# Performance work log

Measured on AMD Instinct MI355X. Metric: run time of the kernel, lower is better.

Reference implementation:

```python
import jax, jax.numpy as jnp
import numpy as np

N = 50000      # nodes per graph
E = 800000     # edges per graph (avg degree 16)
IN = 128       # in_channels == hidden_channels
HID = 128      # out_channels (heads=1)
R = 8          # num_relations
NEG = 0.2      # PyG RGATConv default negative_slope


def setup_inputs() -> dict:
    key = jax.random.key(0)
    ks = jax.random.split(key, 14)
    s_w = (2.0 / (IN + HID)) ** 0.5  # glorot-ish scale
    return {
        "x_one": jax.random.normal(ks[0], (N, IN), jnp.float32),
        "edge_index_one": jax.random.randint(ks[1], (2, E), 0, N),
        "edge_type_one": jax.random.randint(ks[2], (E,), 0, R),
        "x_two": jax.random.normal(ks[3], (N, IN), jnp.float32),
        "edge_index_two": jax.random.randint(ks[4], (2, E), 0, N),
        "edge_type_two": jax.random.randint(ks[5], (E,), 0, R),
        "W1": jax.random.normal(ks[6], (R, IN, HID), jnp.float32) * s_w,
        "q1": jax.random.normal(ks[7], (HID, 1), jnp.float32) * s_w,
        "k1": jax.random.normal(ks[8], (HID, 1), jnp.float32) * s_w,
        "b1": jnp.zeros((HID,), jnp.float32),
        "W2": jax.random.normal(ks[9], (R, IN, HID), jnp.float32) * s_w,
        "q2": jax.random.normal(ks[10], (HID, 1), jnp.float32) * s_w,
        "k2": jax.random.normal(ks[11], (HID, 1), jnp.float32) * s_w,
        "b2": jnp.zeros((HID,), jnp.float32),
    }


def _rgat(x, edge_index, edge_type, W, q, k, b):
    """PyG RGATConv (heads=1, additive-self-attention, across-relation)."""
    n = x.shape[0]
    src, dst = edge_index[0], edge_index[1]
    # per-relation linear transform of all nodes: [R, N, HID]
    xt = jnp.einsum('nd,rdo->rno', x, W)
    out_i = xt[edge_type, dst]   # [E, HID] transformed target (x_i W_r)
    out_j = xt[edge_type, src]   # [E, HID] transformed source (x_j W_r)
    qi = out_i @ q               # [E, 1]
    kj = out_j @ k               # [E, 1]
    alpha = jax.nn.leaky_relu(qi + kj, NEG)
    # scatter-softmax over incoming edges of each dst node
    amax = jax.ops.segment_max(alpha, dst, num_segments=n)
    amax = jnp.where(jnp.isfinite(amax), amax, 0.0)
    ex = jnp.exp(alpha - amax[dst])
    denom = jax.ops.segment_sum(ex, dst, num_segments=n) + 1e-16
    a = ex / denom[dst]          # [E, 1]
    # weighted scatter-add aggregation + bias
    out = jax.ops.segment_sum(a * out_j, dst, num_segments=n) + b
    return out


def reference(x_one, edge_index_one, edge_type_one,
              x_two, edge_index_two, edge_type_two,
              W1, q1, k1, b1, W2, q2, k2, b2):
    o1 = jax.nn.relu(_rgat(x_one, edge_index_one, edge_type_one, W1, q1, k1, b1))
    o2 = jax.nn.relu(_rgat(x_two, edge_index_two, edge_type_two, W2, q2, k2, b2))
    return (o1, o2)
```

## Files before the change

### kernel.cpp

```cpp
#include <hip/hip_runtime.h>


typedef unsigned short u16;
typedef __attribute__((ext_vector_type(8))) short short8;
typedef __attribute__((ext_vector_type(4))) float floatx4;
typedef __attribute__((ext_vector_type(4))) float float4v;
typedef __attribute__((ext_vector_type(4))) unsigned uint4v;

#define BCAP 8192

__device__ __forceinline__ u16 f2bf(float f) {
  union { float f; unsigned u; } v; v.f = f;
  unsigned r = v.u + 0x7FFFu + ((v.u >> 16) & 1u);
  return (u16)(r >> 16);
}
__device__ __forceinline__ float bflo(unsigned v) {
  union { unsigned u; float f; } c; c.u = v << 16; return c.f;
}
__device__ __forceinline__ float bfhi(unsigned v) {
  union { unsigned u; float f; } c; c.u = v & 0xffff0000u; return c.f;
}
__device__ __forceinline__ unsigned cvtpk(float lo, float hi) {
  unsigned r;
  asm("v_cvt_pk_bf16_f32 %0, %1, %2" : "=v"(r) : "v"(lo), "v"(hi));
  return r;
}

__global__ void __launch_bounds__(256) k_prep(
    const float* __restrict__ W1, const float* __restrict__ q1,
    const float* __restrict__ k1, const float* __restrict__ W2,
    const float* __restrict__ q2, const float* __restrict__ k2,
    u16* __restrict__ Wb, u16* __restrict__ Bqk, int* __restrict__ bcnt,
    int KK, int wbHalf) {
  int b = blockIdx.x, tid = threadIdx.x;
  int wbBlocks = 2 * wbHalf;
  if (b < wbBlocks) {
    int gy = b >= wbHalf;
    int t = (b - gy * wbHalf) * 256 + tid;
    int lane = t & 63, nt = (t >> 6) & 7, kk = t >> 9;
    if (kk >= KK) return;
    const float* W = gy ? W2 : W1;
    u16* out = Wb + (size_t)gy * KK * 4096;
    int q = lane >> 4, m16 = lane & 15;
    int c = nt * 16 + m16;
    short8 v;
#pragma unroll
    for (int j = 0; j < 8; ++j) {
      int k = kk * 32 + q * 8 + j;
      v[j] = (short)f2bf(W[(size_t)k * 128 + c]);
    }
    *(short8*)(out + (size_t)t * 8) = v;
  } else {
    int bb = b - wbBlocks;
    if (bb < 2) {
      int z = bb * 256 + tid;
      bcnt[z] = 0;
    }
    int idx = bb * 256 + tid;
    int j = idx & 7, lane = (idx >> 3) & 63, kk = (idx >> 9) & 3, g = idx >> 11;
    int k = kk * 32 + ((lane >> 4) & 3) * 8 + j;
    int n = lane & 15;
    const float* W = g ? W2 : W1;
    const float* vec = (n < 8) ? (g ? q2 : q1) : (g ? k2 : k1);
    const float* row = W + ((size_t)(n & 7) * 128 + k) * 128;
    float s = 0.f;
#pragma unroll
    for (int o = 0; o < 128; o += 4) {
      float4v wv = *(const float4v*)(row + o);
      float4v qv = *(const float4v*)(vec + o);
      s += wv.x * qv.x + wv.y * qv.y + wv.z * qv.z + wv.w * qv.w;
    }
    Bqk[idx] = f2bf(s);
  }
}

struct BinSmem {
  int hist[512];
  int basev[512];
  int runstart[512];
  unsigned sta[8192];
};
union SortGemmSmem {
  BinSmem bn;
  u16 st[4][2][2048];
};

__global__ void __launch_bounds__(256) k_sortgemm(
    const int* __restrict__ ei1, const int* __restrict__ et1,
    const int* __restrict__ ei2, const int* __restrict__ et2,
    int* __restrict__ bcnt, uint2* __restrict__ staged,
    const float* __restrict__ x, const u16* __restrict__ Wb,
    const u16* __restrict__ Bqk, u16* __restrict__ xt,
    float* __restrict__ sq, float* __restrict__ sk,
    int N, int E, int NB, int R, int nbin, int gx) {
  __shared__ SortGemmSmem sm;
  int tid = threadIdx.x;

  if ((int)blockIdx.x < nbin) {
    int* hist = sm.bn.hist;
    int* basev = sm.bn.basev;
    int* runstart = sm.bn.runstart;
    unsigned* sta = sm.bn.sta;
    int E2 = 2 * E;
    int e0 = blockIdx.x * 4096;
    int cnt2 = min(4096, E2 - e0);
    for (int i = tid; i < 512; i += 256) hist[i] = 0;
    __syncthreads();
    int dstg[16], srcet[16], rank[16];
#pragma unroll
    for (int j = 0; j < 16; ++j) {
      int e = e0 + j * 256 + tid;
      dstg[j] = -1;
      if (e < E2) {
        int g = e >= E;
        int el = e - (g ? E : 0);
        const int* ei = g ? ei2 : ei1;
        int s = ei[el], d = ei[E + el];
        int etv = (g ? et2 : et1)[el];
        dstg[j] = g * N + d;
        srcet[j] = (s << 3) | etv;
        rank[j] = atomicAdd(&hist[dstg[j] >> 8], 1);
      }
    }
    __syncthreads();
    basev[tid] = hist[tid];
    basev[tid + 256] = hist[tid + 256];
    __syncthreads();
    for (int off = 1; off < 512; off <<= 1) {
      int i0 = tid, i1 = tid + 256;
      int v0 = (i0 >= off) ? basev[i0 - off] : 0;
      int v1 = (i1 >= off) ? basev[i1 - off] : 0;
      __syncthreads();
      basev[i0] += v0; basev[i1] += v1;
      __syncthreads();
    }
    for (int i = tid; i < NB; i += 256)
      if (hist[i] > 0) runstart[i] = atomicAdd(&bcnt[i], hist[i]);
    __syncthreads();
#pragma unroll
    for (int j = 0; j < 16; ++j)
      if (dstg[j] >= 0) {
        int b = dstg[j] >> 8;
        int slot = basev[b] - hist[b] + rank[j];
        sta[slot * 2] = (unsigned)dstg[j];
        sta[slot * 2 + 1] = (unsigned)srcet[j];
      }
    __syncthreads();
    for (int i = tid; i < cnt2; i += 256) {
      unsigned dg = sta[i * 2], se = sta[i * 2 + 1];
      int b = (int)(dg >> 8);
      int dest = (b << 13) + runstart[b] + (i - (basev[b] - hist[b]));
      staged[dest] = make_uint2(dg, se);
    }
    return;
  }

  int f = blockIdx.x - nbin;
  int bx = f % gx;
  int by = f / gx;
  int wave = tid >> 6, lane = tid & 63;
  int m0 = bx * 64 + wave * 16;
  int rbase = by * 4;
  int q = lane >> 4, m16 = lane & 15;
  int node = m0 + m16;
  int srow = (node < N) ? node : N - 1;
  short8 bfrag[4];
#pragma unroll
  for (int kk = 0; kk < 4; ++kk) {
    const float* ap = x + (size_t)srow * 128 + kk * 32 + q * 8;
    float4v f0 = *(const float4v*)ap;
    float4v f1 = *(const float4v*)(ap + 4);
    union { unsigned u[4]; short8 s; } pb;
    pb.u[0] = cvtpk(f0.x, f0.y); pb.u[1] = cvtpk(f0.z, f0.w);
    pb.u[2] = cvtpk(f1.x, f1.y); pb.u[3] = cvtpk(f1.z, f1.w);
    bfrag[kk] = pb.s;
  }
  if (by == 0) {
    floatx4 accq = (floatx4){0.f, 0.f, 0.f, 0.f};
#pragma unroll
    for (int kk = 0; kk < 4; ++kk) {
      short8 aq = *(const short8*)(Bqk + (size_t)kk * 512 + lane * 8);
      accq = __builtin_amdgcn_mfma_f32_16x16x32_bf16(aq, bfrag[kk], accq, 0, 0, 0);
    }
    if (node < N) {
      float* dst = (q < 2 ? sq : sk) + (size_t)node * 8 + (q & 1) * 4;
      *(float4v*)dst = (float4v){accq[0], accq[1], accq[2], accq[3]};
    }
  }
#pragma unroll
  for (int rr = 0; rr < 4; ++rr) {
    int r = rbase + rr;
    u16* s = sm.st[wave][rr & 1];
    floatx4 acc[8];
#pragma unroll
    for (int nt = 0; nt < 8; ++nt) acc[nt] = (floatx4){0.f, 0.f, 0.f, 0.f};
#pragma unroll
    for (int kk = 0; kk < 4; ++kk) {
      const u16* wbp = Wb + ((size_t)((r * 4 + kk) * 8) * 64 + lane) * 8;
#pragma unroll
      for (int nt = 0; nt < 8; ++nt) {
        short8 a = *(const short8*)(wbp + nt * 512);
        acc[nt] = __builtin_amdgcn_mfma_f32_16x16x32_bf16(a, bfrag[kk], acc[nt], 0, 0, 0);
      }
    }
#pragma unroll
    for (int nt = 0; nt < 8; ++nt) {
      union { unsigned u[2]; unsigned long long ull; } pk;
      pk.u[0] = cvtpk(acc[nt][0], acc[nt][1]);
      pk.u[1] = cvtpk(acc[nt][2], acc[nt][3]);
      int c16 = 2 * nt + (q >> 1);
      *(unsigned long long*)(s + (((m16 << 4) + (c16 ^ m16)) << 3) + ((q & 1) << 2)) = pk.ull;
    }
#pragma unroll
    for (int it = 0; it < 4; ++it) {
      int rl = it * 4 + q;
      int gm = m0 + rl;
      if (gm < N) {
        uint4v vv = *(const uint4v*)(s + (((rl << 4) + (m16 ^ rl)) << 3));
        *(uint4v*)(xt + ((size_t)r * N + gm) * 128 + m16 * 8) = vv;
      }
    }
  }
}

__global__ void __launch_bounds__(256) k_scatter3(
    const uint2* __restrict__ staged, const int* __restrict__ bcnt,
    int* __restrict__ offs, int* __restrict__ ends, int* __restrict__ csr,
    int N2) {
  __shared__ int hist[256];
  __shared__ int sd[256];
  __shared__ int cur[256];
  int b = blockIdx.x, tid = threadIdx.x;
  int nb0 = b << 8;
  int nnode = min(256, N2 - nb0);
  int s0 = b << 13;
  int cnt = bcnt[b];
  hist[tid] = 0;
  __syncthreads();
  for (int i = tid; i < cnt; i += 256)
    atomicAdd(&hist[(int)staged[s0 + i].x - nb0], 1);
  __syncthreads();
  int v = hist[tid];
  sd[tid] = v; __syncthreads();
  for (int off = 1; off < 256; off <<= 1) {
    int t = (tid >= off) ? sd[tid - off] : 0;
    __syncthreads();
    sd[tid] += t;
    __syncthreads();
  }
  int ex = sd[tid] - v;
  if (tid < nnode) {
    offs[nb0 + tid] = s0 + ex;
    ends[nb0 + tid] = s0 + ex + v;
  }
  cur[tid] = ex;
  __syncthreads();
  for (int i = tid; i < cnt; i += 256) {
    uint2 en = staged[s0 + i];
    int node = (int)en.x - nb0;
    int sl = atomicAdd(&cur[node], 1);
    csr[s0 + sl] = (int)en.y;
  }
}

__global__ void __launch_bounds__(256) k_gemm_xt(
    const float* __restrict__ x, const u16* __restrict__ Wb,
    const u16* __restrict__ Bqk, u16* __restrict__ xt,
    float* __restrict__ sq, float* __restrict__ sk,
    int N, int R, int node_base) {
  __shared__ u16 st[4][2][2048];
  int wave = threadIdx.x >> 6, lane = threadIdx.x & 63;
  int m0 = blockIdx.x * 64 + wave * 16;
  int rbase = blockIdx.y * 4;
  int q = lane >> 4, m16 = lane & 15;
  int node = m0 + m16;
  int srow = (node < N) ? node : N - 1;
  short8 bfrag[4];
#pragma unroll
  for (int kk = 0; kk < 4; ++kk) {
    const float* ap = x + (size_t)srow * 128 + kk * 32 + q * 8;
    float4v f0 = *(const float4v*)ap;
    float4v f1 = *(const float4v*)(ap + 4);
    union { unsigned u[4]; short8 s; } pb;
    pb.u[0] = cvtpk(f0.x, f0.y); pb.u[1] = cvtpk(f0.z, f0.w);
    pb.u[2] = cvtpk(f1.x, f1.y); pb.u[3] = cvtpk(f1.z, f1.w);
    bfrag[kk] = pb.s;
  }
  if (blockIdx.y == 0) {
    floatx4 accq = (floatx4){0.f, 0.f, 0.f, 0.f};
#pragma unroll
    for (int kk = 0; kk < 4; ++kk) {
      short8 aq = *(const short8*)(Bqk + (size_t)kk * 512 + lane * 8);
      accq = __builtin_amdgcn_mfma_f32_16x16x32_bf16(aq, bfrag[kk], accq, 0, 0, 0);
    }
    if (node < N) {
      float* dst = (q < 2 ? sq : sk) + (size_t)(node_base + node) * 8 + (q & 1) * 4;
      *(float4v*)dst = (float4v){accq[0], accq[1], accq[2], accq[3]};
    }
  }
#pragma unroll
  for (int rr = 0; rr < 4; ++rr) {
    int r = rbase + rr;
    u16* s = st[wave][rr & 1];
    floatx4 acc[8];
#pragma unroll
    for (int nt = 0; nt < 8; ++nt) acc[nt] = (floatx4){0.f, 0.f, 0.f, 0.f};
#pragma unroll
    for (int kk = 0; kk < 4; ++kk) {
      const u16* wbp = Wb + ((size_t)((r * 4 + kk) * 8) * 64 + lane) * 8;
#pragma unroll
      for (int nt = 0; nt < 8; ++nt) {
        short8 a = *(const short8*)(wbp + nt * 512);
        acc[nt] = __builtin_amdgcn_mfma_f32_16x16x32_bf16(a, bfrag[kk], acc[nt], 0, 0, 0);
      }
    }
#pragma unroll
    for (int nt = 0; nt < 8; ++nt) {
      union { unsigned u[2]; unsigned long long ull; } pk;
      pk.u[0] = cvtpk(acc[nt][0], acc[nt][1]);
      pk.u[1] = cvtpk(acc[nt][2], acc[nt][3]);
      int c16 = 2 * nt + (q >> 1);
      *(unsigned long long*)(s + (((m16 << 4) + (c16 ^ m16)) << 3) + ((q & 1) << 2)) = pk.ull;
    }
#pragma unroll
    for (int it = 0; it < 4; ++it) {
      int rl = it * 4 + q;
      int gm = m0 + rl;
      if (gm < N) {
        uint4v vv = *(const uint4v*)(s + (((rl << 4) + (m16 ^ rl)) << 3));
        *(uint4v*)(xt + ((size_t)r * N + gm) * 128 + m16 * 8) = vv;
      }
    }
  }
}

__global__ void __launch_bounds__(256) k_aggregate(
    const int* __restrict__ csr, const int* __restrict__ offs,
    const int* __restrict__ ends,
    const float* __restrict__ sq, const float* __restrict__ sk,
    const u16* __restrict__ xt, const float* __restrict__ bias,
    float* __restrict__ out, int N, int node_base) {
  int nl = blockIdx.x * 4 + (threadIdx.x >> 6);
  int lane = threadIdx.x & 63;
  if (nl >= N) return;
  int node = node_base + nl;
  int start = offs[node], end = ends[node];
  const float* sqn = sq + (size_t)node * 8;

  float al[8]; int pl[8];
  float m = -INFINITY;
  {
    int c = 0;
    for (int i = start + lane; i < end; i += 64, ++c) {
      int p = csr[i]; int s = p >> 3, e = p & 7;
      float a = sqn[e] + sk[(size_t)(node_base + s) * 8 + e];
      a = (a > 0.f) ? a : 0.2f * a;
      if (c < 8) { al[c] = a; pl[c] = p; }
      m = fmaxf(m, a);
    }
  }
#pragma unroll
  for (int off = 32; off; off >>= 1) m = fmaxf(m, __shfl_xor(m, off));

  float ssum = 0.f;
  {
    int c = 0;
    for (int i = start + lane; i < end; i += 64, ++c) {
      float a;
      if (c < 8) a = al[c];
      else {
        int p = csr[i]; int s = p >> 3, e = p & 7;
        a = sqn[e] + sk[(size_t)(node_base + s) * 8 + e];
        a = (a > 0.f) ? a : 0.2f * a;
      }
      ssum += __expf(a - m);
    }
  }
#pragma unroll
  for (int off = 32; off; off >>= 1) ssum += __shfl_xor(ssum, off);
  float inv = 1.f / (ssum + 1e-16f);

  float acc0 = 0.f, acc1 = 0.f;
  const char* xtb = (const char*)xt;
  int c = 0;
  for (int base = start; base < end; base += 64, ++c) {
    int cnt = min(64, end - base);
    float w = 0.f; int b = 0;
    {
      int i = base + lane;
      if (i < end) {
        int p; float a;
        if (c < 8) { p = pl[c]; a = al[c]; }
        else {
          p = csr[i]; int s = p >> 3, e = p & 7;
          a = sqn[e] + sk[(size_t)(node_base + s) * 8 + e];
          a = (a > 0.f) ? a : 0.2f * a;
        }
        w = __expf(a - m) * inv;
        b = ((p & 7) * N + (p >> 3)) << 8;
      }
    }
    int j = 0;
    for (; j + 3 < cnt; j += 4) {
      float w0 = __shfl(w, j), w1 = __shfl(w, j + 1),
            w2 = __shfl(w, j + 2), w3 = __shfl(w, j + 3);
      int b0 = __shfl(b, j), b1 = __shfl(b, j + 1),
          b2 = __shfl(b, j + 2), b3 = __shfl(b, j + 3);
      unsigned v0 = *(const unsigned*)(xtb + b0 + lane * 4);
      unsigned v1 = *(const unsigned*)(xtb + b1 + lane * 4);
      unsigned v2 = *(const unsigned*)(xtb + b2 + lane * 4);
      unsigned v3 = *(const unsigned*)(xtb + b3 + lane * 4);
      acc0 += w0 * bflo(v0); acc1 += w0 * bfhi(v0);
      acc0 += w1 * bflo(v1); acc1 += w1 * bfhi(v1);
      acc0 += w2 * bflo(v2); acc1 += w2 * bfhi(v2);
      acc0 += w3 * bflo(v3); acc1 += w3 * bfhi(v3);
    }
    for (; j < cnt; ++j) {
      float w0 = __shfl(w, j);
      int b0 = __shfl(b, j);
      unsigned v0 = *(const unsigned*)(xtb + b0 + lane * 4);
      acc0 += w0 * bflo(v0); acc1 += w0 * bfhi(v0);
    }
  }
  float o0 = fmaxf(acc0 + bias[lane * 2], 0.f);
  float o1 = fmaxf(acc1 + bias[lane * 2 + 1], 0.f);
  union { float f[2]; unsigned long long u; } pk;
  pk.f[0] = o0; pk.f[1] = o1;
  __builtin_nontemporal_store(pk.u,
      (unsigned long long*)(out + (size_t)nl * 128 + lane * 2));
}

extern "C" void kernel_launch(void* const* d_in, const int* in_sizes, int n_in,
                              void* d_out, int out_size, void* d_ws, size_t ws_size,
                              hipStream_t stream) {
  const float* x1 = (const float*)d_in[0];
  const int* ei1 = (const int*)d_in[1];
  const int* et1 = (const int*)d_in[2];
  const float* x2 = (const float*)d_in[3];
  const int* ei2 = (const int*)d_in[4];
  const int* et2 = (const int*)d_in[5];
  const float* W1 = (const float*)d_in[6];
  const float* q1 = (const float*)d_in[7];
  const float* k1 = (const float*)d_in[8];
  const float* b1 = (const float*)d_in[9];
  const float* W2 = (const float*)d_in[10];
  const float* q2 = (const float*)d_in[11];
  const float* k2 = (const float*)d_in[12];
  const float* b2 = (const float*)d_in[13];

  const int N = in_sizes[0] / 128;
  const int E = in_sizes[1] / 2;
  const int R = in_sizes[6] / (128 * 128);
  const int KK = R * 4;
  const int N2 = 2 * N;
  const int NB = (N2 + 255) >> 8;

  size_t off = 0;
  char* w = (char*)d_ws;
  auto carve = [&](size_t bytes) -> void* {
    void* p = w + off;
    off += (bytes + 255) & ~(size_t)255;
    return p;
  };
  u16* Wb = (u16*)carve((size_t)2 * KK * 4096 * 2);
  u16* Bqk = (u16*)carve((size_t)2 * 4 * 64 * 8 * 2);
  float* sq = (float*)carve((size_t)N2 * 8 * 4);
  float* sk = (float*)carve((size_t)N2 * 8 * 4);
  int* offs = (int*)carve((size_t)N2 * 4);
  int* ends = (int*)carve((size_t)N2 * 4);
  int* bcnt = (int*)carve(512 * 4);
  int* csr = (int*)carve((size_t)NB * BCAP * 4);
  uint2* staged = (uint2*)carve((size_t)NB * BCAP * 8);
  u16* xt = (u16*)carve((size_t)R * N * 128 * 2);
  if (off > ws_size) return;

  const int nbin = (2 * E + 4095) / 4096;
  const int gx = (N + 63) / 64;
  const int wbHalf = (KK * 512 + 255) / 256;

  k_prep<<<dim3(2 * wbHalf + 16), dim3(256), 0, stream>>>(
      W1, q1, k1, W2, q2, k2, Wb, Bqk, bcnt, KK, wbHalf);
  k_sortgemm<<<dim3(nbin + 2 * gx), dim3(256), 0, stream>>>(
      ei1, et1, ei2, et2, bcnt, staged,
      x1, Wb, Bqk, xt, sq, sk, N, E, NB, R, nbin, gx);
  k_scatter3<<<dim3(NB), dim3(256), 0, stream>>>(staged, bcnt, offs, ends, csr, N2);
  k_aggregate<<<dim3((N + 3) / 4), dim3(256), 0, stream>>>(
      csr, offs, ends, sq, sk, xt, b1, (float*)d_out, N, 0);
  k_gemm_xt<<<dim3(gx, 2), dim3(256), 0, stream>>>(
      x2, Wb + (size_t)KK * 4096, Bqk + 2048, xt, sq, sk, N, R, N);
  k_aggregate<<<dim3((N + 3) / 4), dim3(256), 0, stream>>>(
      csr, offs, ends, sq, sk, xt, b2,
      (float*)d_out + (size_t)N * 128, N, N);
}
```

Measured before the change: 324.2 us.

## Overlap graph-two GEMM with graph-one aggregation in a combined launch

The GEMM and aggregation bodies move into shared device functions, and a new combined kernel runs the graph-two per-relation transform blocks alongside the graph-one aggregation blocks. The graph-two xt buffer is placed where the staging buffer was, which is free once scatter has finished, so the two stages no longer serialise on one buffer. This saves one launch and lets compute-bound MFMA work overlap the memory-bound gather. If the workspace is too small it falls back to the old sequential path.

```diff
diff --git a/kernel.cpp b/kernel.cpp
--- a/kernel.cpp
+++ b/kernel.cpp
@@ -85,6 +85,171 @@
   u16 st[4][2][2048];
 };
 
+__device__ __forceinline__ void gemm_body(
+    u16 st[4][2][2048], int bx, int by, int tid,
+    const float* __restrict__ x, const u16* __restrict__ Wb,
+    const u16* __restrict__ Bqk, u16* __restrict__ xt,
+    float* __restrict__ sq, float* __restrict__ sk,
+    int N, int node_base) {
+  int wave = tid >> 6, lane = tid & 63;
+  int m0 = bx * 64 + wave * 16;
+  int rbase = by * 4;
+  int q = lane >> 4, m16 = lane & 15;
+  int node = m0 + m16;
+  int srow = (node < N) ? node : N - 1;
+  short8 bfrag[4];
+#pragma unroll
+  for (int kk = 0; kk < 4; ++kk) {
+    const float* ap = x + (size_t)srow * 128 + kk * 32 + q * 8;
+    float4v f0 = *(const float4v*)ap;
+    float4v f1 = *(const float4v*)(ap + 4);
+    union { unsigned u[4]; short8 s; } pb;
+    pb.u[0] = cvtpk(f0.x, f0.y); pb.u[1] = cvtpk(f0.z, f0.w);
+    pb.u[2] = cvtpk(f1.x, f1.y); pb.u[3] = cvtpk(f1.z, f1.w);
+    bfrag[kk] = pb.s;
+  }
+  if (by == 0) {
+    floatx4 accq = (floatx4){0.f, 0.f, 0.f, 0.f};
+#pragma unroll
+    for (int kk = 0; kk < 4; ++kk) {
+      short8 aq = *(const short8*)(Bqk + (size_t)kk * 512 + lane * 8);
+      accq = __builtin_amdgcn_mfma_f32_16x16x32_bf16(aq, bfrag[kk], accq, 0, 0, 0);
+    }
+    if (node < N) {
+      float* dst = (q < 2 ? sq : sk) + (size_t)(node_base + node) * 8 + (q & 1) * 4;
+      *(float4v*)dst = (float4v){accq[0], accq[1], accq[2], accq[3]};
+    }
+  }
+#pragma unroll
+  for (int rr = 0; rr < 4; ++rr) {
+    int r = rbase + rr;
+    u16* s = st[tid >> 6][rr & 1];
+    floatx4 acc[8];
+#pragma unroll
+    for (int nt = 0; nt < 8; ++nt) acc[nt] = (floatx4){0.f, 0.f, 0.f, 0.f};
+#pragma unroll
+    for (int kk = 0; kk < 4; ++kk) {
+      const u16* wbp = Wb + ((size_t)((r * 4 + kk) * 8) * 64 + lane) * 8;
+#pragma unroll
+      for (int nt = 0; nt < 8; ++nt) {
+        short8 a = *(const short8*)(wbp + nt * 512);
+        acc[nt] = __builtin_amdgcn_mfma_f32_16x16x32_bf16(a, bfrag[kk], acc[nt], 0, 0, 0);
+      }
+    }
+#pragma unroll
+    for (int nt = 0; nt < 8; ++nt) {
+      union { unsigned u[2]; unsigned long long ull; } pk;
+      pk.u[0] = cvtpk(acc[nt][0], acc[nt][1]);
+      pk.u[1] = cvtpk(acc[nt][2], acc[nt][3]);
+      int c16 = 2 * nt + (q >> 1);
+      *(unsigned long long*)(s + (((m16 << 4) + (c16 ^ m16)) << 3) + ((q & 1) << 2)) = pk.ull;
+    }
+#pragma unroll
+    for (int it = 0; it < 4; ++it) {
+      int rl = it * 4 + q;
+      int gm = m0 + rl;
+      if (gm < N) {
+        uint4v vv = *(const uint4v*)(s + (((rl << 4) + (m16 ^ rl)) << 3));
+        *(uint4v*)(xt + ((size_t)r * N + gm) * 128 + m16 * 8) = vv;
+      }
+    }
+  }
+}
+
+__device__ __forceinline__ void agg_body(
+    int nl, int lane,
+    const int* __restrict__ csr, const int* __restrict__ offs,
+    const int* __restrict__ ends,
+    const float* __restrict__ sq, const float* __restrict__ sk,
+    const u16* __restrict__ xt, const float* __restrict__ bias,
+    float* __restrict__ out, int N, int node_base) {
+  int node = node_base + nl;
+  int start = offs[node], end = ends[node];
+  const float* sqn = sq + (size_t)node * 8;
+
+  float al[8]; int pl[8];
+  float m = -INFINITY;
+  {
+    int c = 0;
+    for (int i = start + lane; i < end; i += 64, ++c) {
+      int p = csr[i]; int s = p >> 3, e = p & 7;
+      float a = sqn[e] + sk[(size_t)(node_base + s) * 8 + e];
+      a = (a > 0.f) ? a : 0.2f * a;
+      if (c < 8) { al[c] = a; pl[c] = p; }
+      m = fmaxf(m, a);
+    }
+  }
+#pragma unroll
+  for (int off = 32; off; off >>= 1) m = fmaxf(m, __shfl_xor(m, off));
+
+  float ssum = 0.f;
+  {
+    int c = 0;
+    for (int i = start + lane; i < end; i += 64, ++c) {
+      float a;
+      if (c < 8) a = al[c];
+      else {
+        int p = csr[i]; int s = p >> 3, e = p & 7;
+        a = sqn[e] + sk[(size_t)(node_base + s) * 8 + e];
+        a = (a > 0.f) ? a : 0.2f * a;
+      }
+      ssum += __expf(a - m);
+    }
+  }
+#pragma unroll
+  for (int off = 32; off; off >>= 1) ssum += __shfl_xor(ssum, off);
+  float inv = 1.f / (ssum + 1e-16f);
+
+  float acc0 = 0.f, acc1 = 0.f;
+  const char* xtb = (const char*)xt;
+  int c = 0;
+  for (int base = start; base < end; base += 64, ++c) {
+    int cnt = min(64, end - base);
+    float w = 0.f; int b = 0;
+    {
+      int i = base + lane;
+      if (i < end) {
+        int p; float a;
+        if (c < 8) { p = pl[c]; a = al[c]; }
+        else {
+          p = csr[i]; int s = p >> 3, e = p & 7;
+          a = sqn[e] + sk[(size_t)(node_base + s) * 8 + e];
+          a = (a > 0.f) ? a : 0.2f * a;
+        }
+        w = __expf(a - m) * inv;
+        b = ((p & 7) * N + (p >> 3)) << 8;
+      }
+    }
+    int j = 0;
+    for (; j + 3 < cnt; j += 4) {
+      float w0 = __shfl(w, j), w1 = __shfl(w, j + 1),
+            w2 = __shfl(w, j + 2), w3 = __shfl(w, j + 3);
+      int b0 = __shfl(b, j), b1 = __shfl(b, j + 1),
+          b2 = __shfl(b, j + 2), b3 = __shfl(b, j + 3);
+      unsigned v0 = *(const unsigned*)(xtb + b0 + lane * 4);
+      unsigned v1 = *(const unsigned*)(xtb + b1 + lane * 4);
+      unsigned v2 = *(const unsigned*)(xtb + b2 + lane * 4);
+      unsigned v3 = *(const unsigned*)(xtb + b3 + lane * 4);
+      acc0 += w0 * bflo(v0); acc1 += w0 * bfhi(v0);
+      acc0 += w1 * bflo(v1); acc1 += w1 * bfhi(v1);
+      acc0 += w2 * bflo(v2); acc1 += w2 * bfhi(v2);
+      acc0 += w3 * bflo(v3); acc1 += w3 * bfhi(v3);
+    }
+    for (; j < cnt; ++j) {
+      float w0 = __shfl(w, j);
+      int b0 = __shfl(b, j);
+      unsigned v0 = *(const unsigned*)(xtb + b0 + lane * 4);
+      acc0 += w0 * bflo(v0); acc1 += w0 * bfhi(v0);
+    }
+  }
+  float o0 = fmaxf(acc0 + bias[lane * 2], 0.f);
+  float o1 = fmaxf(acc1 + bias[lane * 2 + 1], 0.f);
+  union { float f[2]; unsigned long long u; } pk;
+  pk.f[0] = o0; pk.f[1] = o1;
+  __builtin_nontemporal_store(pk.u,
+      (unsigned long long*)(out + (size_t)nl * 128 + lane * 2));
+}
+
 __global__ void __launch_bounds__(256) k_sortgemm(
     const int* __restrict__ ei1, const int* __restrict__ et1,
     const int* __restrict__ ei2, const int* __restrict__ et2,
@@ -154,73 +319,8 @@
     }
     return;
   }
-
   int f = blockIdx.x - nbin;
-  int bx = f % gx;
-  int by = f / gx;
-  int wave = tid >> 6, lane = tid & 63;
-  int m0 = bx * 64 + wave * 16;
-  int rbase = by * 4;
-  int q = lane >> 4, m16 = lane & 15;
-  int node = m0 + m16;
-  int srow = (node < N) ? node : N - 1;
-  short8 bfrag[4];
-#pragma unroll
-  for (int kk = 0; kk < 4; ++kk) {
-    const float* ap = x + (size_t)srow * 128 + kk * 32 + q * 8;
-    float4v f0 = *(const float4v*)ap;
-    float4v f1 = *(const float4v*)(ap + 4);
-    union { unsigned u[4]; short8 s; } pb;
-    pb.u[0] = cvtpk(f0.x, f0.y); pb.u[1] = cvtpk(f0.z, f0.w);
-    pb.u[2] = cvtpk(f1.x, f1.y); pb.u[3] = cvtpk(f1.z, f1.w);
-    bfrag[kk] = pb.s;
-  }
-  if (by == 0) {
-    floatx4 accq = (floatx4){0.f, 0.f, 0.f, 0.f};
-#pragma unroll
-    for (int kk = 0; kk < 4; ++kk) {
-      short8 aq = *(const short8*)(Bqk + (size_t)kk * 512 + lane * 8);
-      accq = __builtin_amdgcn_mfma_f32_16x16x32_bf16(aq, bfrag[kk], accq, 0, 0, 0);
-    }
-    if (node < N) {
-      float* dst = (q < 2 ? sq : sk) + (size_t)node * 8 + (q & 1) * 4;
-      *(float4v*)dst = (float4v){accq[0], accq[1], accq[2], accq[3]};
-    }
-  }
-#pragma unroll
-  for (int rr = 0; rr < 4; ++rr) {
-    int r = rbase + rr;
-    u16* s = sm.st[wave][rr & 1];
-    floatx4 acc[8];
-#pragma unroll
-    for (int nt = 0; nt < 8; ++nt) acc[nt] = (floatx4){0.f, 0.f, 0.f, 0.f};
-#pragma unroll
-    for (int kk = 0; kk < 4; ++kk) {
-      const u16* wbp = Wb + ((size_t)((r * 4 + kk) * 8) * 64 + lane) * 8;
-#pragma unroll
-      for (int nt = 0; nt < 8; ++nt) {
-        short8 a = *(const short8*)(wbp + nt * 512);
-        acc[nt] = __builtin_amdgcn_mfma_f32_16x16x32_bf16(a, bfrag[kk], acc[nt], 0, 0, 0);
-      }
-    }
-#pragma unroll
-    for (int nt = 0; nt < 8; ++nt) {
-      union { unsigned u[2]; unsigned long long ull; } pk;
-      pk.u[0] = cvtpk(acc[nt][0], acc[nt][1]);
-      pk.u[1] = cvtpk(acc[nt][2], acc[nt][3]);
-      int c16 = 2 * nt + (q >> 1);
-      *(unsigned long long*)(s + (((m16 << 4) + (c16 ^ m16)) << 3) + ((q & 1) << 2)) = pk.ull;
-    }
-#pragma unroll
-    for (int it = 0; it < 4; ++it) {
-      int rl = it * 4 + q;
-      int gm = m0 + rl;
-      if (gm < N) {
-        uint4v vv = *(const uint4v*)(s + (((rl << 4) + (m16 ^ rl)) << 3));
-        *(uint4v*)(xt + ((size_t)r * N + gm) * 128 + m16 * 8) = vv;
-      }
-    }
-  }
+  gemm_body(sm.st, f % gx, f / gx, tid, x, Wb, Bqk, xt, sq, sk, N, 0);
 }
 
 __global__ void __launch_bounds__(256) k_scatter3(
@@ -263,75 +363,36 @@
   }
 }
 
+__global__ void __launch_bounds__(256) k_aggemm(
+    const int* __restrict__ csr, const int* __restrict__ offs,
+    const int* __restrict__ ends,
+    const float* __restrict__ sq, const float* __restrict__ sk,
+    const u16* __restrict__ xt0, const float* __restrict__ b1,
+    float* __restrict__ out,
+    const float* __restrict__ x2, const u16* __restrict__ Wb1,
+    const u16* __restrict__ Bqk1, u16* __restrict__ xt1,
+    float* __restrict__ sqw, float* __restrict__ skw,
+    int N, int R, int gx) {
+  __shared__ u16 st[4][2][2048];
+  int tid = threadIdx.x;
+  if ((int)blockIdx.x < 2 * gx) {
+    int f = blockIdx.x;
+    gemm_body(st, f % gx, f / gx, tid, x2, Wb1, Bqk1, xt1, sqw, skw, N, N);
+    return;
+  }
+  int nl = (blockIdx.x - 2 * gx) * 4 + (tid >> 6);
+  if (nl >= N) return;
+  agg_body(nl, tid & 63, csr, offs, ends, sq, sk, xt0, b1, out, N, 0);
+}
+
 __global__ void __launch_bounds__(256) k_gemm_xt(
     const float* __restrict__ x, const u16* __restrict__ Wb,
     const u16* __restrict__ Bqk, u16* __restrict__ xt,
     float* __restrict__ sq, float* __restrict__ sk,
     int N, int R, int node_base) {
   __shared__ u16 st[4][2][2048];
-  int wave = threadIdx.x >> 6, lane = threadIdx.x & 63;
-  int m0 = blockIdx.x * 64 + wave * 16;
-  int rbase = blockIdx.y * 4;
-  int q = lane >> 4, m16 = lane & 15;
-  int node = m0 + m16;
-  int srow = (node < N) ? node : N - 1;
-  short8 bfrag[4];
-#pragma unroll
-  for (int kk = 0; kk < 4; ++kk) {
-    const float* ap = x + (size_t)srow * 128 + kk * 32 + q * 8;
-    float4v f0 = *(const float4v*)ap;
-    float4v f1 = *(const float4v*)(ap + 4);
-    union { unsigned u[4]; short8 s; } pb;
-    pb.u[0] = cvtpk(f0.x, f0.y); pb.u[1] = cvtpk(f0.z, f0.w);
-    pb.u[2] = cvtpk(f1.x, f1.y); pb.u[3] = cvtpk(f1.z, f1.w);
-    bfrag[kk] = pb.s;
-  }
-  if (blockIdx.y == 0) {
-    floatx4 accq = (floatx4){0.f, 0.f, 0.f, 0.f};
-#pragma unroll
-    for (int kk = 0; kk < 4; ++kk) {
-      short8 aq = *(const short8*)(Bqk + (size_t)kk * 512 + lane * 8);
-      accq = __builtin_amdgcn_mfma_f32_16x16x32_bf16(aq, bfrag[kk], accq, 0, 0, 0);
-    }
-    if (node < N) {
-      float* dst = (q < 2 ? sq : sk) + (size_t)(node_base + node) * 8 + (q & 1) * 4;
-      *(float4v*)dst = (float4v){accq[0], accq[1], accq[2], accq[3]};
-    }
-  }
-#pragma unroll
-  for (int rr = 0; rr < 4; ++rr) {
-    int r = rbase + rr;
-    u16* s = st[wave][rr & 1];
-    floatx4 acc[8];
-#pragma unroll
-    for (int nt = 0; nt < 8; ++nt) acc[nt] = (floatx4){0.f, 0.f, 0.f, 0.f};
-#pragma unroll
-    for (int kk = 0; kk < 4; ++kk) {
-      const u16* wbp = Wb + ((size_t)((r * 4 + kk) * 8) * 64 + lane) * 8;
-#pragma unroll
-      for (int nt = 0; nt < 8; ++nt) {
-        short8 a = *(const short8*)(wbp + nt * 512);
-        acc[nt] = __builtin_amdgcn_mfma_f32_16x16x32_bf16(a, bfrag[kk], acc[nt], 0, 0, 0);
-      }
-    }
-#pragma unroll
-    for (int nt = 0; nt < 8; ++nt) {
-      union { unsigned u[2]; unsigned long long ull; } pk;
-      pk.u[0] = cvtpk(acc[nt][0], acc[nt][1]);
-      pk.u[1] = cvtpk(acc[nt][2], acc[nt][3]);
-      int c16 = 2 * nt + (q >> 1);
-      *(unsigned long long*)(s + (((m16 << 4) + (c16 ^ m16)) << 3) + ((q & 1) << 2)) = pk.ull;
-    }
-#pragma unroll
-    for (int it = 0; it < 4; ++it) {
-      int rl = it * 4 + q;
-      int gm = m0 + rl;
-      if (gm < N) {
-        uint4v vv = *(const uint4v*)(s + (((rl << 4) + (m16 ^ rl)) << 3));
-        *(uint4v*)(xt + ((size_t)r * N + gm) * 128 + m16 * 8) = vv;
-      }
-    }
-  }
+  gemm_body(st, blockIdx.x, blockIdx.y, threadIdx.x, x, Wb, Bqk, xt, sq, sk,
+            N, node_base);
 }
 
 __global__ void __launch_bounds__(256) k_aggregate(
@@ -341,93 +402,9 @@
     const u16* __restrict__ xt, const float* __restrict__ bias,
     float* __restrict__ out, int N, int node_base) {
   int nl = blockIdx.x * 4 + (threadIdx.x >> 6);
-  int lane = threadIdx.x & 63;
   if (nl >= N) return;
-  int node = node_base + nl;
-  int start = offs[node], end = ends[node];
-  const float* sqn = sq + (size_t)node * 8;
-
-  float al[8]; int pl[8];
-  float m = -INFINITY;
-  {
-    int c = 0;
-    for (int i = start + lane; i < end; i += 64, ++c) {
-      int p = csr[i]; int s = p >> 3, e = p & 7;
-      float a = sqn[e] + sk[(size_t)(node_base + s) * 8 + e];
-      a = (a > 0.f) ? a : 0.2f * a;
-      if (c < 8) { al[c] = a; pl[c] = p; }
-      m = fmaxf(m, a);
-    }
-  }
-#pragma unroll
-  for (int off = 32; off; off >>= 1) m = fmaxf(m, __shfl_xor(m, off));
-
-  float ssum = 0.f;
-  {
-    int c = 0;
-    for (int i = start + lane; i < end; i += 64, ++c) {
-      float a;
-      if (c < 8) a = al[c];
-      else {
-        int p = csr[i]; int s = p >> 3, e = p & 7;
-        a = sqn[e] + sk[(size_t)(node_base + s) * 8 + e];
-        a = (a > 0.f) ? a : 0.2f * a;
-      }
-      ssum += __expf(a - m);
-    }
-  }
-#pragma unroll
-  for (int off = 32; off; off >>= 1) ssum += __shfl_xor(ssum, off);
-  float inv = 1.f / (ssum + 1e-16f);
-
-  float acc0 = 0.f, acc1 = 0.f;
-  const char* xtb = (const char*)xt;
-  int c = 0;
-  for (int base = start; base < end; base += 64, ++c) {
-    int cnt = min(64, end - base);
-    float w = 0.f; int b = 0;
-    {
-      int i = base + lane;
-      if (i < end) {
-        int p; float a;
-        if (c < 8) { p = pl[c]; a = al[c]; }
-        else {
-          p = csr[i]; int s = p >> 3, e = p & 7;
-          a = sqn[e] + sk[(size_t)(node_base + s) * 8 + e];
-          a = (a > 0.f) ? a : 0.2f * a;
-        }
-        w = __expf(a - m) * inv;
-        b = ((p & 7) * N + (p >> 3)) << 8;
-      }
-    }
-    int j = 0;
-    for (; j + 3 < cnt; j += 4) {
-      float w0 = __shfl(w, j), w1 = __shfl(w, j + 1),
-            w2 = __shfl(w, j + 2), w3 = __shfl(w, j + 3);
-      int b0 = __shfl(b, j), b1 = __shfl(b, j + 1),
-          b2 = __shfl(b, j + 2), b3 = __shfl(b, j + 3);
-      unsigned v0 = *(const unsigned*)(xtb + b0 + lane * 4);
-      unsigned v1 = *(const unsigned*)(xtb + b1 + lane * 4);
-      unsigned v2 = *(const unsigned*)(xtb + b2 + lane * 4);
-      unsigned v3 = *(const unsigned*)(xtb + b3 + lane * 4);
-      acc0 += w0 * bflo(v0); acc1 += w0 * bfhi(v0);
-      acc0 += w1 * bflo(v1); acc1 += w1 * bfhi(v1);
-      acc0 += w2 * bflo(v2); acc1 += w2 * bfhi(v2);
-      acc0 += w3 * bflo(v3); acc1 += w3 * bfhi(v3);
-    }
-    for (; j < cnt; ++j) {
-      float w0 = __shfl(w, j);
-      int b0 = __shfl(b, j);
-      unsigned v0 = *(const unsigned*)(xtb + b0 + lane * 4);
-      acc0 += w0 * bflo(v0); acc1 += w0 * bfhi(v0);
-    }
-  }
-  float o0 = fmaxf(acc0 + bias[lane * 2], 0.f);
-  float o1 = fmaxf(acc1 + bias[lane * 2 + 1], 0.f);
-  union { float f[2]; unsigned long long u; } pk;
-  pk.f[0] = o0; pk.f[1] = o1;
-  __builtin_nontemporal_store(pk.u,
-      (unsigned long long*)(out + (size_t)nl * 128 + lane * 2));
+  agg_body(nl, threadIdx.x & 63, csr, offs, ends, sq, sk, xt, bias, out, N,
+           node_base);
 }
 
 extern "C" void kernel_launch(void* const* d_in, const int* in_sizes, int n_in,
@@ -470,25 +447,40 @@
   int* ends = (int*)carve((size_t)N2 * 4);
   int* bcnt = (int*)carve(512 * 4);
   int* csr = (int*)carve((size_t)NB * BCAP * 4);
+  u16* xt0 = (u16*)carve((size_t)R * N * 128 * 2);
+  size_t staged_off = off;
   uint2* staged = (uint2*)carve((size_t)NB * BCAP * 8);
-  u16* xt = (u16*)carve((size_t)R * N * 128 * 2);
   if (off > ws_size) return;
+  size_t xt_bytes = (size_t)R * N * 128 * 2;
+  bool dual = (staged_off + xt_bytes) <= ws_size;
+  u16* xt1 = dual ? (u16*)(w + staged_off) : xt0;
 
   const int nbin = (2 * E + 4095) / 4096;
   const int gx = (N + 63) / 64;
   const int wbHalf = (KK * 512 + 255) / 256;
+  const int na = (N + 3) / 4;
 
   k_prep<<<dim3(2 * wbHalf + 16), dim3(256), 0, stream>>>(
       W1, q1, k1, W2, q2, k2, Wb, Bqk, bcnt, KK, wbHalf);
   k_sortgemm<<<dim3(nbin + 2 * gx), dim3(256), 0, stream>>>(
       ei1, et1, ei2, et2, bcnt, staged,
-      x1, Wb, Bqk, xt, sq, sk, N, E, NB, R, nbin, gx);
+      x1, Wb, Bqk, xt0, sq, sk, N, E, NB, R, nbin, gx);
   k_scatter3<<<dim3(NB), dim3(256), 0, stream>>>(staged, bcnt, offs, ends, csr, N2);
-  k_aggregate<<<dim3((N + 3) / 4), dim3(256), 0, stream>>>(
-      csr, offs, ends, sq, sk, xt, b1, (float*)d_out, N, 0);
-  k_gemm_xt<<<dim3(gx, 2), dim3(256), 0, stream>>>(
-      x2, Wb + (size_t)KK * 4096, Bqk + 2048, xt, sq, sk, N, R, N);
-  k_aggregate<<<dim3((N + 3) / 4), dim3(256), 0, stream>>>(
-      csr, offs, ends, sq, sk, xt, b2,
-      (float*)d_out + (size_t)N * 128, N, N);
-}
+
+  if (dual) {
+    k_aggemm<<<dim3(2 * gx + na), dim3(256), 0, stream>>>(
+        csr, offs, ends, sq, sk, xt0, b1, (float*)d_out,
+        x2, Wb + (size_t)KK * 4096, Bqk + 2048, xt1, sq, sk, N, R, gx);
+    k_aggregate<<<dim3(na), dim3(256), 0, stream>>>(
+        csr, offs, ends, sq, sk, xt1, b2,
+        (float*)d_out + (size_t)N * 128, N, N);
+  } else {
+    k_aggregate<<<dim3(na), dim3(256), 0, stream>>>(
+        csr, offs, ends, sq, sk, xt0, b1, (float*)d_out, N, 0);
+    k_gemm_xt<<<dim3(gx, 2), dim3(256), 0, stream>>>(
+        x2, Wb + (size_t)KK * 4096, Bqk + 2048, xt0, sq, sk, N, R, N);
+    k_aggregate<<<dim3(na), dim3(256), 0, stream>>>(
+        csr, offs, ends, sq, sk, xt0, b2,
+        (float*)d_out + (size_t)N * 128, N, N);
+  }
+}
```

After: 361.9 us. 11.6% more time.
